# Kernel tuning notes

Measured on AMD Instinct MI355X. Metric: run time of the kernel, lower is better.

The kernel has to match this reference:

```python
import jax, jax.numpy as jnp
import numpy as np

N = 100000   # n_nodes
E = 1000000  # n_edges
B = 2000     # batch of interactions
K = 20       # n_neighbors
D = 172      # memory/node/edge/embedding dim
T = 172      # time encoding dim
MSG = 2 * D + D + T  # 688, identity message function
HEADS = 2


def setup_inputs() -> dict:
    key = jax.random.key(0)
    ks = jax.random.split(key, 32)
    g = lambda i, shape, fan: jax.random.normal(ks[i], shape, jnp.float32) / np.float32(np.sqrt(fan))
    inp = {}
    inp['memory'] = jax.random.normal(ks[0], (N, D), jnp.float32)
    inp['messages'] = jax.random.normal(ks[1], (N, MSG), jnp.float32)
    inp['edge_features'] = jax.random.normal(ks[2], (E, D), jnp.float32)
    inp['edge_times'] = jax.random.uniform(ks[3], (B,), jnp.float32) * 10000.0
    inp['neighbor_times'] = jax.random.uniform(ks[4], (3 * B, K), jnp.float32) * 10000.0
    # TimeEncode init: w = 1 / 10^linspace(0, 9, T)
    inp['time_w'] = jnp.asarray(1.0 / 10.0 ** np.linspace(0, 9, T), jnp.float32)
    inp['time_b'] = jnp.zeros((T,), jnp.float32)
    # GRUCell params
    inp['gru_w_ih'] = g(5, (3 * D, MSG), MSG)
    inp['gru_w_hh'] = g(6, (3 * D, D), D)
    inp['gru_b_ih'] = jnp.zeros((3 * D,), jnp.float32)
    inp['gru_b_hh'] = jnp.zeros((3 * D,), jnp.float32)
    # temporal attention params: query = [feat||time], key = [feat||edge||time]
    inp['w_q'] = g(7, (D, D + T), D + T)
    inp['w_k'] = g(8, (D, D + D + T), D + D + T)
    inp['w_v'] = g(9, (D, D + D + T), D + D + T)
    inp['w_o'] = g(10, (D, D), D)
    # MergeLayer(attn_out, src_feat)
    inp['merge_w1'] = g(11, (D, 2 * D), 2 * D)
    inp['merge_b1'] = jnp.zeros((D,), jnp.float32)
    inp['merge_w2'] = g(12, (D, D), D)
    inp['merge_b2'] = jnp.zeros((D,), jnp.float32)
    # affinity MergeLayer -> scalar score
    inp['aff_w1'] = g(13, (D, 2 * D), 2 * D)
    inp['aff_b1'] = jnp.zeros((D,), jnp.float32)
    inp['aff_w2'] = g(14, (1, D), D)
    inp['aff_b2'] = jnp.zeros((1,), jnp.float32)
    inp['source_nodes'] = jax.random.randint(ks[15], (B,), 0, N, jnp.int32)
    inp['destination_nodes'] = jax.random.randint(ks[16], (B,), 0, N, jnp.int32)
    inp['negative_nodes'] = jax.random.randint(ks[17], (B,), 0, N, jnp.int32)
    inp['neighbors'] = jax.random.randint(ks[18], (3 * B, K), 0, N, jnp.int32)
    inp['neighbor_edge_idxs'] = jax.random.randint(ks[19], (3 * B, K), 0, E, jnp.int32)
    return inp


def reference(memory, messages, edge_features, edge_times, neighbor_times,
              time_w, time_b, gru_w_ih, gru_w_hh, gru_b_ih, gru_b_hh,
              w_q, w_k, w_v, w_o, merge_w1, merge_b1, merge_w2, merge_b2,
              aff_w1, aff_b1, aff_w2, aff_b2,
              source_nodes, destination_nodes, negative_nodes,
              neighbors, neighbor_edge_idxs):
    d = memory.shape[1]
    dh = d // HEADS
    k_nbr = neighbors.shape[1]

    def time_enc(t):  # TimeEncode: cos(t * w + b)
        return jnp.cos(t[..., None] * time_w + time_b)

    # --- GRU memory update from aggregated ('last') messages ---
    gi = messages @ gru_w_ih.T + gru_b_ih          # [N, 3D]
    gh = memory @ gru_w_hh.T + gru_b_hh            # [N, 3D]
    i_r, i_z, i_n = jnp.split(gi, 3, axis=-1)
    h_r, h_z, h_n = jnp.split(gh, 3, axis=-1)
    r = jax.nn.sigmoid(i_r + h_r)
    z = jax.nn.sigmoid(i_z + h_z)
    n = jnp.tanh(i_n + r * h_n)
    mem_upd = (1.0 - z) * n + z * memory           # [N, D]

    # --- temporal graph attention embedding (1 layer) ---
    nodes = jnp.concatenate([source_nodes, destination_nodes, negative_nodes])  # [3B]
    ts = jnp.concatenate([edge_times, edge_times, edge_times])                  # [3B]
    m = nodes.shape[0]
    src_feat = mem_upd[nodes]                                                   # [3B, D]
    q_in = jnp.concatenate([src_feat, time_enc(jnp.zeros_like(ts))], axis=-1)   # [3B, D+T]
    nbr_feat = mem_upd[neighbors]                                               # [3B, K, D]
    e_feat = edge_features[neighbor_edge_idxs]                                  # [3B, K, D]
    dt = ts[:, None] - neighbor_times                                           # [3B, K]
    k_in = jnp.concatenate([nbr_feat, e_feat, time_enc(dt)], axis=-1)           # [3B, K, 2D+T]

    q = (q_in @ w_q.T).reshape(m, HEADS, dh)
    kk = (k_in @ w_k.T).reshape(m, k_nbr, HEADS, dh)
    vv = (k_in @ w_v.T).reshape(m, k_nbr, HEADS, dh)
    scores = jnp.einsum('nhd,nkhd->nhk', q, kk) / np.float32(np.sqrt(dh))
    valid = (neighbors > 0)[:, None, :]            # node 0 is the pad node
    scores = jnp.where(valid, scores, jnp.float32(-1e9))
    attn = jax.nn.softmax(scores, axis=-1)
    ctx = jnp.einsum('nhk,nkhd->nhd', attn, vv).reshape(m, d) @ w_o.T
    h1 = jax.nn.relu(jnp.concatenate([ctx, src_feat], axis=-1) @ merge_w1.T + merge_b1)
    emb = h1 @ merge_w2.T + merge_b2               # [3B, D]

    # --- affinity score on (src,dst) and (src,neg) pairs ---
    b = source_nodes.shape[0]
    s_emb, d_emb, n_emb = emb[:b], emb[b:2 * b], emb[2 * b:]
    s_cat = jnp.concatenate([s_emb, s_emb], axis=0)
    d_cat = jnp.concatenate([d_emb, n_emb], axis=0)
    ah = jax.nn.relu(jnp.concatenate([s_cat, d_cat], axis=-1) @ aff_w1.T + aff_b1)
    prob = jax.nn.sigmoid((ah @ aff_w2.T + aff_b2).squeeze(-1))  # [2B]
    return prob[:b], prob[b:]
```

## Files before the change

kernel.cpp:

```cpp
#include <hip/hip_runtime.h>
#include <math.h>

#define N_NODES 100000
#define BATCH   2000
#define KNBR    20
#define DF      172
#define MSGD    688
#define M3      6000
#define DH      86
#define KIN_D   516

#define KA      864
#define JP      768
#define KREAL   860
#define KSTEPS  (KA / 32)
#define NTILES_N ((N_NODES + 127) / 128)
#define NWG_GRU (NTILES_N * 6)

#define NKV     120000
#define KP_KV   544
#define JKV     384
#define KVS     352
#define NKV_TILES ((NKV + 127) / 128)

typedef __bf16 bf16x8 __attribute__((ext_vector_type(8)));
typedef __bf16 bf16x4 __attribute__((ext_vector_type(4)));
typedef float  f32x4  __attribute__((ext_vector_type(4)));

#define WPB_OFF   0
#define BP4_OFF   331776
#define WKV_OFF   332544
#define MU_OFF    436992
#define UNI_OFF   17636992
#define KV_OFF    UNI_OFF
#define QB_OFF    38756992
#define CAT_OFF   39286400
#define EMBB_OFF  40922752
#define MW1O_OFF  41812608
#define WQB_OFF   41842192
#define WM1B_OFF  41875984
#define WM2B_OFF  41909776
#define WAFFB_OFF 41928208
#define BM1P_OFF  41962000
#define BM2P_OFF  41962192
#define BAFFP_OFF 41962384
#define NODES_OFF 41962768

__device__ __forceinline__ float sigmoidf_(float x) { return 1.0f / (1.0f + expf(-x)); }

typedef __attribute__((address_space(1))) const void gvoid;
typedef __attribute__((address_space(3))) void svoid;
__device__ __forceinline__ void gl16(const void* g, void* l) {
    __builtin_amdgcn_global_load_lds((gvoid*)g, (svoid*)l, 16, 0, 0);
}

__global__ __launch_bounds__(256) void prep_kernel(
    const float* __restrict__ w_ih, const float* __restrict__ w_hh,
    const float* __restrict__ b_ih, const float* __restrict__ b_hh,
    __bf16* __restrict__ wpb, float* __restrict__ bp4)
{
    int idx = blockIdx.x * 256 + threadIdx.x;
    if (idx < JP * KA) {
        int j = idx / KA, k = idx - j * KA;
        int d = j >> 2, g = j & 3;
        float v = 0.f;
        if (d < DF) {
            if (g == 0) {
                if (k < MSGD) v = w_ih[d * MSGD + k];
                else if (k < KREAL) v = w_hh[d * DF + (k - MSGD)];
            } else if (g == 1) {
                if (k < MSGD) v = w_ih[(d + DF) * MSGD + k];
                else if (k < KREAL) v = w_hh[(d + DF) * DF + (k - MSGD)];
            } else if (g == 2) {
                if (k < MSGD) v = w_ih[(d + 2 * DF) * MSGD + k];
            } else {
                if (k >= MSGD && k < KREAL) v = w_hh[(d + 2 * DF) * DF + (k - MSGD)];
            }
        }
        wpb[idx] = (__bf16)v;
    }
    if (idx < JP) {
        int d = idx >> 2, g = idx & 3;
        float b = 0.f;
        if (d < DF) {
            if (g == 0) b = b_ih[d] + b_hh[d];
            else if (g == 1) b = b_ih[d + DF] + b_hh[d + DF];
            else if (g == 2) b = b_ih[d + 2 * DF];
            else            b = b_hh[d + 2 * DF];
        }
        bp4[idx] = b;
    }
}

__global__ __launch_bounds__(256) void prep_kv_kernel(
    const float* __restrict__ w_k, const float* __restrict__ w_v,
    __bf16* __restrict__ wkvb)
{
    int idx = blockIdx.x * 256 + threadIdx.x;
    if (idx < JKV * KP_KV) {
        int j = idx / KP_KV, k = idx - j * KP_KV;
        float v = 0.f;
        if (k < KIN_D) {
            if (j < DF) v = w_k[j * KIN_D + k];
            else if (j >= 192 && j < 192 + DF) v = w_v[(j - 192) * KIN_D + k];
        }
        wkvb[idx] = (__bf16)v;
    }
}

__global__ __launch_bounds__(256) void conv_kernel(
    const float* __restrict__ messages, const float* __restrict__ memory,
    __bf16* __restrict__ xb)
{
    const long total = (long)N_NODES * (KA / 8);
    for (long idx = (long)blockIdx.x * 256 + threadIdx.x; idx < total;
         idx += (long)gridDim.x * 256) {
        const int r  = (int)(idx / (KA / 8));
        const int k  = (int)(idx - (long)r * (KA / 8)) * 8;
        float f[8];
        if (k < MSGD) {
            const float4 a = *(const float4*)(messages + (size_t)r * MSGD + k);
            const float4 b = *(const float4*)(messages + (size_t)r * MSGD + k + 4);
            f[0]=a.x; f[1]=a.y; f[2]=a.z; f[3]=a.w;
            f[4]=b.x; f[5]=b.y; f[6]=b.z; f[7]=b.w;
        } else {
            const int o = k - MSGD;
            const float4 a = *(const float4*)(memory + (size_t)r * DF + o);
            float4 b = make_float4(0.f, 0.f, 0.f, 0.f);
            if (o <= 164) b = *(const float4*)(memory + (size_t)r * DF + o + 4);
            f[0]=a.x; f[1]=a.y; f[2]=a.z; f[3]=a.w;
            f[4]=b.x; f[5]=b.y; f[6]=b.z; f[7]=b.w;
        }
        bf16x8 v;
#pragma unroll
        for (int j = 0; j < 8; ++j) v[j] = (__bf16)f[j];
        *(bf16x8*)(xb + (size_t)r * KA + k) = v;
    }
}

__global__ __launch_bounds__(256) void mw1o_kernel(
    const float* __restrict__ merge_w1, const float* __restrict__ w_o,
    float* __restrict__ mw1o)
{
    int idx = blockIdx.x * 256 + threadIdx.x;
    if (idx >= DF * DF) return;
    int j = idx / DF, k = idx - j * DF;
    float s = 0.f;
    for (int c = 0; c < DF; ++c)
        s = fmaf(merge_w1[j * 344 + c], w_o[c * DF + k], s);
    mw1o[idx] = s;
}

__global__ __launch_bounds__(256) void prep_tail_kernel(
    const float* __restrict__ w_q, const float* __restrict__ mw1o,
    const float* __restrict__ merge_w1, const float* __restrict__ merge_w2,
    const float* __restrict__ aff_w1,
    const float* __restrict__ merge_b1, const float* __restrict__ merge_b2,
    const float* __restrict__ aff_b1,
    const int* __restrict__ src_nodes, const int* __restrict__ dst_nodes,
    const int* __restrict__ neg_nodes,
    __bf16* __restrict__ wqb, __bf16* __restrict__ wm1b,
    __bf16* __restrict__ wm2b, __bf16* __restrict__ waffb,
    float* __restrict__ bm1p, float* __restrict__ bm2p,
    float* __restrict__ baffp, int* __restrict__ nodes_cat)
{
    int idx = blockIdx.x * 256 + threadIdx.x;
    if (idx < 192 * 352) {
        int j = idx / 352, k = idx - j * 352;
        float vq = 0.f, vm = 0.f, va = 0.f;
        if (j < DF) {
            if (k < DF) {
                vq = w_q[j * 344 + k];
                vm = mw1o[j * DF + k];
                va = aff_w1[j * 344 + k];
            } else if (k >= 176 && k < 348) {
                vq = w_q[j * 344 + 172 + (k - 176)];
                vm = merge_w1[j * 344 + 172 + (k - 176)];
                va = aff_w1[j * 344 + 172 + (k - 176)];
            }
        }
        wqb[idx] = (__bf16)vq;
        wm1b[idx] = (__bf16)vm;
        waffb[idx] = (__bf16)va;
    }
    if (idx < 192 * 192) {
        int j = idx / 192, k = idx - j * 192;
        wm2b[idx] = (__bf16)((j < DF && k < DF) ? merge_w2[j * DF + k] : 0.f);
    }
    if (idx < 192) {
        bm1p[idx]  = (idx < DF) ? merge_b1[idx] : 0.f;
        bm2p[idx]  = (idx < DF) ? merge_b2[idx] : 0.f;
        baffp[idx] = (idx < DF) ? aff_b1[idx] : 0.f;
    }
    if (idx < 6016) {
        int i = min(idx, M3 - 1);
        int node;
        if (i < BATCH)          node = src_nodes[i];
        else if (i < 2 * BATCH) node = dst_nodes[i - BATCH];
        else                    node = neg_nodes[i - 2 * BATCH];
        nodes_cat[idx] = node;
    }
}

__global__ __launch_bounds__(256) void gru_mfma3_kernel(
    const __bf16* __restrict__ xb, const __bf16* __restrict__ wpb,
    const float* __restrict__ bp4, const float* __restrict__ memory,
    __bf16* __restrict__ mem_upd)
{
    __shared__ __align__(16) __bf16 Ws[3][128 * 32];
    __shared__ __align__(16) __bf16 Xs[3][128 * 32];

    const int t    = threadIdx.x;
    const int w    = t >> 6, lane = t & 63;
    const int lo   = lane & 15, hi = lane >> 4;
    const int wm   = w >> 1, wn = w & 1;

    const int orig = blockIdx.x;
    const int q = NWG_GRU >> 3, rr = NWG_GRU & 7;
    const int xcd = orig & 7, oidx = orig >> 3;
    const int wgid = (xcd < rr ? xcd * (q + 1) : rr * (q + 1) + (xcd - rr) * q) + oidx;
    const int m_tile = wgid % 6;
    const int n_tile = wgid / 6;
    const int n0 = n_tile * 128;
    const int j0 = m_tile * 128;

    const int srow  = lane >> 2;
    const int sslot = ((lane & 3) ^ ((lane >> 3) & 3)) * 8;

    f32x4 acc[4][4];
#pragma unroll
    for (int mi = 0; mi < 4; ++mi)
#pragma unroll
        for (int ni = 0; ni < 4; ++ni)
            acc[mi][ni] = (f32x4){0.f, 0.f, 0.f, 0.f};

    const __bf16* wbase = wpb + (size_t)j0 * KA;
    const __bf16* xbase = xb + (size_t)n0 * KA;

#define STAGE(buf, k0)                                                          \
    {                                                                           \
        _Pragma("unroll")                                                       \
        for (int qq = 0; qq < 2; ++qq) {                                        \
            const int lr = w * 32 + qq * 16 + srow;                             \
            gl16(wbase + (size_t)lr * KA + (k0) + sslot,                        \
                 &Ws[buf][(w * 32 + qq * 16) * 32]);                            \
            gl16(xbase + (size_t)lr * KA + (k0) + sslot,                        \
                 &Xs[buf][(w * 32 + qq * 16) * 32]);                            \
        }                                                                       \
    }

    STAGE(0, 0);
    STAGE(1, 32);

    const int fsa = (hi ^ ((lo >> 1) & 3)) * 8;
    for (int ks = 0; ks < KSTEPS; ++ks) {
        if (ks < KSTEPS - 1) {
            asm volatile("s_waitcnt vmcnt(4)" ::: "memory");
        } else {
            asm volatile("s_waitcnt vmcnt(0)" ::: "memory");
        }
        __builtin_amdgcn_s_barrier();
        if (ks + 2 < KSTEPS) STAGE((ks + 2) % 3, (ks + 2) * 32);

        const int bi = ks % 3;
        bf16x8 af[4], bx_[4];
#pragma unroll
        for (int i = 0; i < 4; ++i) {
            af[i]  = *(const bf16x8*)&Ws[bi][(wm * 64 + i * 16 + lo) * 32 + fsa];
            bx_[i] = *(const bf16x8*)&Xs[bi][(wn * 64 + i * 16 + lo) * 32 + fsa];
        }
#pragma unroll
        for (int mi = 0; mi < 4; ++mi)
#pragma unroll
            for (int ni = 0; ni < 4; ++ni)
                acc[mi][ni] = __builtin_amdgcn_mfma_f32_16x16x32_bf16(
                    af[mi], bx_[ni], acc[mi][ni], 0, 0, 0);
    }
#undef STAGE

    const int dbase = m_tile * 32 + wm * 16;
#pragma unroll
    for (int mi = 0; mi < 4; ++mi) {
        const int d = dbase + mi * 4 + hi;
        if (d >= DF) continue;
        const float4 b4 = *(const float4*)&bp4[4 * d];
#pragma unroll
        for (int ni = 0; ni < 4; ++ni) {
            const int n = n0 + wn * 64 + ni * 16 + lo;
            if (n >= N_NODES) continue;
            float sr  = acc[mi][ni][0] + b4.x;
            float sz  = acc[mi][ni][1] + b4.y;
            float gin = acc[mi][ni][2] + b4.z;
            float ghn = acc[mi][ni][3] + b4.w;
            float mem = memory[(size_t)n * DF + d];
            float rg  = sigmoidf_(sr);
            float zg  = sigmoidf_(sz);
            float nt  = tanhf(fmaf(rg, ghn, gin));
            mem_upd[(size_t)n * DF + d] = (__bf16)fmaf(zg, mem - nt, nt);
        }
    }
}

__global__ __launch_bounds__(256) void kv_gemm3_kernel(
    const __bf16* __restrict__ mem_upd, const float* __restrict__ edge_features,
    const float* __restrict__ edge_times, const float* __restrict__ neighbor_times,
    const float* __restrict__ time_w, const float* __restrict__ time_b,
    const int* __restrict__ neighbors, const int* __restrict__ nbr_eidx,
    const __bf16* __restrict__ wkvb, __bf16* __restrict__ kv)
{
    __shared__ __align__(16) __bf16 Ws[128][32];
    __shared__ __align__(16) __bf16 Xs[128][32];

    const int t    = threadIdx.x;
    const int w    = t >> 6, lane = t & 63;
    const int lo   = lane & 15, hi = lane >> 4;
    const int wm   = w >> 1, wn = w & 1;

    const int bx     = blockIdx.x;
    const int n_tile = bx / 3;
    const int m_tile = bx - n_tile * 3;
    const int n0     = n_tile * 128;
    const int j0     = m_tile * 128;

    const int xrow  = t >> 1, xhalf = t & 1;
    const int nr    = min(n0 + xrow, NKV - 1);
    const int nbr   = neighbors[nr];
    const int eidx  = nbr_eidx[nr];
    const float dt  = edge_times[(nr / KNBR) % BATCH] - neighbor_times[nr];
    const __bf16* mrow = mem_upd       + (size_t)nbr  * DF;
    const float*  erow = edge_features + (size_t)eidx * DF;
    const __bf16* wrow = wkvb + (size_t)(j0 + xrow) * KP_KV;

    f32x4 acc[4][4];
#pragma unroll
    for (int mi = 0; mi < 4; ++mi)
#pragma unroll
        for (int ni = 0; ni < 4; ++ni)
            acc[mi][ni] = (f32x4){0.f, 0.f, 0.f, 0.f};

#define LOADX(k0, xh, xf)                                                       \
    {                                                                           \
        _Pragma("unroll")                                                       \
        for (int c = 0; c < 4; ++c) {                                           \
            const int kb = (k0) + xhalf * 16 + c * 4;                           \
            if (kb < DF) {                                                      \
                xh[c] = *(const bf16x4*)(mrow + kb);                            \
            } else if (kb < 2 * DF) {                                           \
                xf[c] = *(const float4*)(erow + (kb - DF));                     \
            } else if (kb < KIN_D) {                                            \
                const float4 tw = *(const float4*)(time_w + (kb - 2 * DF));     \
                const float4 tb = *(const float4*)(time_b + (kb - 2 * DF));     \
                float4 v;                                                       \
                v.x = cosf(fmaf(dt, tw.x, tb.x));                               \
                v.y = cosf(fmaf(dt, tw.y, tb.y));                               \
                v.z = cosf(fmaf(dt, tw.z, tb.z));                               \
                v.w = cosf(fmaf(dt, tw.w, tb.w));                               \
                xf[c] = v;                                                      \
            } else {                                                            \
                xf[c] = make_float4(0.f, 0.f, 0.f, 0.f);                        \
            }                                                                   \
        }                                                                       \
    }

    bf16x4 xh[4];
    float4 xf[4];
    bf16x8 wp0, wp1;
    LOADX(0, xh, xf);
    wp0 = *(const bf16x8*)(wrow + xhalf * 16);
    wp1 = *(const bf16x8*)(wrow + xhalf * 16 + 8);

    for (int ks = 0; ks < KP_KV / 32; ++ks) {
        const int k0 = ks * 32;
        bf16x8 x0, x1;
#pragma unroll
        for (int c = 0; c < 4; ++c) {
            const int kb = k0 + xhalf * 16 + c * 4;
            __bf16 e0, e1, e2, e3;
            if (kb < DF) {
                e0 = xh[c][0]; e1 = xh[c][1]; e2 = xh[c][2]; e3 = xh[c][3];
            } else {
                e0 = (__bf16)xf[c].x; e1 = (__bf16)xf[c].y;
                e2 = (__bf16)xf[c].z; e3 = (__bf16)xf[c].w;
            }
            if (c < 2) { x0[c*4]=e0; x0[c*4+1]=e1; x0[c*4+2]=e2; x0[c*4+3]=e3; }
            else { x1[(c-2)*4]=e0; x1[(c-2)*4+1]=e1; x1[(c-2)*4+2]=e2; x1[(c-2)*4+3]=e3; }
        }
        *(bf16x8*)&Ws[xrow][xhalf * 16]     = wp0;
        *(bf16x8*)&Ws[xrow][xhalf * 16 + 8] = wp1;
        *(bf16x8*)&Xs[xrow][xhalf * 16]     = x0;
        *(bf16x8*)&Xs[xrow][xhalf * 16 + 8] = x1;

        if (ks + 1 < KP_KV / 32) {
            LOADX(k0 + 32, xh, xf);
            wp0 = *(const bf16x8*)(wrow + k0 + 32 + xhalf * 16);
            wp1 = *(const bf16x8*)(wrow + k0 + 32 + xhalf * 16 + 8);
        }

        asm volatile("s_waitcnt lgkmcnt(0)" ::: "memory");
        __builtin_amdgcn_s_barrier();

        bf16x8 af[4], bx_[4];
#pragma unroll
        for (int i = 0; i < 4; ++i) {
            af[i]  = *(const bf16x8*)&Ws[wm * 64 + i * 16 + lo][hi * 8];
            bx_[i] = *(const bf16x8*)&Xs[wn * 64 + i * 16 + lo][hi * 8];
        }
#pragma unroll
        for (int mi = 0; mi < 4; ++mi)
#pragma unroll
            for (int ni = 0; ni < 4; ++ni)
                acc[mi][ni] = __builtin_amdgcn_mfma_f32_16x16x32_bf16(
                    af[mi], bx_[ni], acc[mi][ni], 0, 0, 0);

        __builtin_amdgcn_s_barrier();
    }
#undef LOADX

#pragma unroll
    for (int mi = 0; mi < 4; ++mi) {
        const int jb = j0 + wm * 64 + mi * 16 + hi * 4;
        int off;
        if (jb + 3 < DF)                 off = jb;
        else if (jb >= 192 && jb < 361)  off = jb - 16;
        else continue;
#pragma unroll
        for (int ni = 0; ni < 4; ++ni) {
            const int n = n0 + wn * 64 + ni * 16 + lo;
            if (n >= NKV) continue;
            bf16x4 o;
            o[0] = (__bf16)acc[mi][ni][0];
            o[1] = (__bf16)acc[mi][ni][1];
            o[2] = (__bf16)acc[mi][ni][2];
            o[3] = (__bf16)acc[mi][ni][3];
            *(bf16x4*)(kv + (size_t)n * KVS + off) = o;
        }
    }
}

__global__ __launch_bounds__(256) void q_gemm_kernel(
    const __bf16* __restrict__ wqb, const __bf16* __restrict__ mem_upd,
    const float* __restrict__ time_b, const int* __restrict__ nodes_cat,
    __bf16* __restrict__ qbuf)
{
    __shared__ __align__(16) __bf16 Ws[128][32];
    __shared__ __align__(16) __bf16 Xs[128][32];

    const int t    = threadIdx.x;
    const int w    = t >> 6, lane = t & 63;
    const int lo   = lane & 15, hi = lane >> 4;
    const int wm   = w >> 1, wn = w & 1;

    const int n_tile = blockIdx.x >> 1;
    const int j0     = (blockIdx.x & 1) * 64;
    const int n0     = n_tile * 128;

    const int xrow  = t >> 1, xhalf = t & 1;
    const int nr    = min(n0 + xrow, M3 - 1);
    const __bf16* mrow = mem_upd + (size_t)nodes_cat[nr] * DF;
    const __bf16* wrow = wqb + (size_t)(j0 + xrow) * 352;

    f32x4 acc[4][4];
#pragma unroll
    for (int mi = 0; mi < 4; ++mi)
#pragma unroll
        for (int ni = 0; ni < 4; ++ni)
            acc[mi][ni] = (f32x4){0.f, 0.f, 0.f, 0.f};

    for (int k0 = 0; k0 < 352; k0 += 32) {
        bf16x8 w0 = *(const bf16x8*)(wrow + k0 + xhalf * 16);
        bf16x8 w1 = *(const bf16x8*)(wrow + k0 + xhalf * 16 + 8);
        bf16x8 x0, x1;
#pragma unroll
        for (int c = 0; c < 4; ++c) {
            const int b = k0 + xhalf * 16 + c * 4;
            __bf16 e0, e1, e2, e3;
            if (b + 3 < DF) {
                bf16x4 h = *(const bf16x4*)(mrow + b);
                e0 = h[0]; e1 = h[1]; e2 = h[2]; e3 = h[3];
            } else if (b >= 176 && b < 348) {
                const float4 tb = *(const float4*)(time_b + (b - 176));
                e0 = (__bf16)cosf(tb.x); e1 = (__bf16)cosf(tb.y);
                e2 = (__bf16)cosf(tb.z); e3 = (__bf16)cosf(tb.w);
            } else {
                e0 = e1 = e2 = e3 = (__bf16)0.f;
            }
            if (c < 2) { x0[c*4]=e0; x0[c*4+1]=e1; x0[c*4+2]=e2; x0[c*4+3]=e3; }
            else { x1[(c-2)*4]=e0; x1[(c-2)*4+1]=e1; x1[(c-2)*4+2]=e2; x1[(c-2)*4+3]=e3; }
        }
        *(bf16x8*)&Ws[xrow][xhalf * 16]     = w0;
        *(bf16x8*)&Ws[xrow][xhalf * 16 + 8] = w1;
        *(bf16x8*)&Xs[xrow][xhalf * 16]     = x0;
        *(bf16x8*)&Xs[xrow][xhalf * 16 + 8] = x1;
        __syncthreads();

        bf16x8 af[4], bx_[4];
#pragma unroll
        for (int i = 0; i < 4; ++i) {
            af[i]  = *(const bf16x8*)&Ws[wm * 64 + i * 16 + lo][hi * 8];
            bx_[i] = *(const bf16x8*)&Xs[wn * 64 + i * 16 + lo][hi * 8];
        }
#pragma unroll
        for (int mi = 0; mi < 4; ++mi)
#pragma unroll
            for (int ni = 0; ni < 4; ++ni)
                acc[mi][ni] = __builtin_amdgcn_mfma_f32_16x16x32_bf16(
                    af[mi], bx_[ni], acc[mi][ni], 0, 0, 0);
        __syncthreads();
    }

#pragma unroll
    for (int mi = 0; mi < 4; ++mi) {
        const int jb = j0 + wm * 64 + mi * 16 + hi * 4;
        if (jb + 3 >= 176) continue;
#pragma unroll
        for (int ni = 0; ni < 4; ++ni) {
            const int n = n0 + wn * 64 + ni * 16 + lo;
            if (n >= M3) continue;
            bf16x4 o;
            o[0]=(__bf16)acc[mi][ni][0]; o[1]=(__bf16)acc[mi][ni][1];
            o[2]=(__bf16)acc[mi][ni][2]; o[3]=(__bf16)acc[mi][ni][3];
            *(bf16x4*)(qbuf + (size_t)n * 176 + jb) = o;
        }
    }
}

__global__ __launch_bounds__(256) void attn_mid_kernel(
    const __bf16* __restrict__ mem_upd, const __bf16* __restrict__ kv,
    const __bf16* __restrict__ qb, const int* __restrict__ neighbors,
    const int* __restrict__ nodes_cat, __bf16* __restrict__ cat)
{
    __shared__ __align__(16) __bf16 kvs[KNBR][KVS];
    __shared__ float qs[176];
    __shared__ float scl[2][KNBR];
    __shared__ float attnl[2][KNBR];
    __shared__ int   nbrs[KNBR];

    const int i = blockIdx.x;
    const int t = threadIdx.x;

    if (t < KNBR) nbrs[t] = neighbors[i * KNBR + t];
    if (t < 176) qs[t] = (float)qb[(size_t)i * 176 + t];
    {
        const uint4* src = (const uint4*)(kv + (size_t)i * KNBR * KVS);
        uint4* dst = (uint4*)&kvs[0][0];
        for (int idx = t; idx < KNBR * KVS / 8; idx += 256) dst[idx] = src[idx];
    }
    __syncthreads();

    if (t < 2 * KNBR) {
        int h = t / KNBR, kn = t - h * KNBR;
        float s = 0.f;
#pragma unroll 2
        for (int j = 0; j < DH; ++j)
            s = fmaf(qs[h * DH + j], (float)kvs[kn][h * DH + j], s);
        s /= sqrtf((float)DH);
        scl[h][kn] = (nbrs[kn] > 0) ? s : -1e9f;
    }
    __syncthreads();
    if (t < 2) {
        float m = -INFINITY;
        for (int kn = 0; kn < KNBR; ++kn) m = fmaxf(m, scl[t][kn]);
        float se = 0.f;
        for (int kn = 0; kn < KNBR; ++kn) se += expf(scl[t][kn] - m);
        float inv = 1.f / se;
        for (int kn = 0; kn < KNBR; ++kn) attnl[t][kn] = expf(scl[t][kn] - m) * inv;
    }
    __syncthreads();
    if (t < DF) {
        int h = t / DH;
        float cx = 0.f;
#pragma unroll
        for (int kn = 0; kn < KNBR; ++kn)
            cx = fmaf(attnl[h][kn], (float)kvs[kn][176 + t], cx);
        cat[(size_t)i * 352 + t] = (__bf16)cx;
        cat[(size_t)i * 352 + 176 + t] = mem_upd[(size_t)nodes_cat[i] * DF + t];
    }
    if (t < 4) {
        cat[(size_t)i * 352 + 172 + t] = (__bf16)0.f;
        cat[(size_t)i * 352 + 348 + t] = (__bf16)0.f;
    }
}

__global__ __launch_bounds__(256) void merge_emb_kernel(
    const __bf16* __restrict__ cat, const __bf16* __restrict__ wm1b,
    const __bf16* __restrict__ wm2b, const float* __restrict__ bm1p,
    const float* __restrict__ bm2p, __bf16* __restrict__ embb)
{
    __shared__ __align__(16) __bf16 Ws[192 * 32];
    __shared__ __align__(16) __bf16 Xs[128 * 32];
    __shared__ __align__(16) __bf16 h1[128 * 200];

    const int t    = threadIdx.x;
    const int w    = t >> 6, lane = t & 63;
    const int lo   = lane & 15, hi = lane >> 4;
    const int wm   = w >> 1, wn = w & 1;
    const int n0   = blockIdx.x * 128;

    const int srow  = lane >> 2;
    const int sslot = ((lane & 3) ^ ((lane >> 3) & 3)) * 8;
    const int fsa   = (hi ^ ((lo >> 1) & 3)) * 8;

    f32x4 acc[6][4];
#pragma unroll
    for (int mi = 0; mi < 6; ++mi)
#pragma unroll
        for (int ni = 0; ni < 4; ++ni)
            acc[mi][ni] = (f32x4){0.f, 0.f, 0.f, 0.f};

    for (int k0 = 0; k0 < 352; k0 += 32) {
#pragma unroll
        for (int qq = 0; qq < 3; ++qq) {
            const int jr = w * 48 + qq * 16 + srow;
            gl16(wm1b + (size_t)jr * 352 + k0 + sslot, &Ws[(w * 48 + qq * 16) * 32]);
        }
#pragma unroll
        for (int qq = 0; qq < 2; ++qq) {
            const int r = w * 32 + qq * 16 + srow;
            const int nr = min(n0 + r, M3 - 1);
            gl16(cat + (size_t)nr * 352 + k0 + sslot, &Xs[(w * 32 + qq * 16) * 32]);
        }
        asm volatile("s_waitcnt vmcnt(0)" ::: "memory");
        __syncthreads();

        bf16x8 af[6], bx_[4];
#pragma unroll
        for (int i = 0; i < 6; ++i)
            af[i] = *(const bf16x8*)&Ws[(wm * 96 + i * 16 + lo) * 32 + fsa];
#pragma unroll
        for (int i = 0; i < 4; ++i)
            bx_[i] = *(const bf16x8*)&Xs[(wn * 64 + i * 16 + lo) * 32 + fsa];
#pragma unroll
        for (int mi = 0; mi < 6; ++mi)
#pragma unroll
            for (int ni = 0; ni < 4; ++ni)
                acc[mi][ni] = __builtin_amdgcn_mfma_f32_16x16x32_bf16(
                    af[mi], bx_[ni], acc[mi][ni], 0, 0, 0);
        __syncthreads();
    }

#pragma unroll
    for (int mi = 0; mi < 6; ++mi) {
        const int jb = wm * 96 + mi * 16 + hi * 4;
        const float4 b4 = *(const float4*)(bm1p + jb);
#pragma unroll
        for (int ni = 0; ni < 4; ++ni) {
            const int nl = wn * 64 + ni * 16 + lo;
            bf16x4 o;
            o[0] = (__bf16)fmaxf(acc[mi][ni][0] + b4.x, 0.f);
            o[1] = (__bf16)fmaxf(acc[mi][ni][1] + b4.y, 0.f);
            o[2] = (__bf16)fmaxf(acc[mi][ni][2] + b4.z, 0.f);
            o[3] = (__bf16)fmaxf(acc[mi][ni][3] + b4.w, 0.f);
            *(bf16x4*)&h1[nl * 200 + jb] = o;
        }
    }
    __syncthreads();

    f32x4 acc2[6][4];
#pragma unroll
    for (int mi = 0; mi < 6; ++mi)
#pragma unroll
        for (int ni = 0; ni < 4; ++ni)
            acc2[mi][ni] = (f32x4){0.f, 0.f, 0.f, 0.f};

    for (int k0 = 0; k0 < 192; k0 += 32) {
#pragma unroll
        for (int qq = 0; qq < 3; ++qq) {
            const int jr = w * 48 + qq * 16 + srow;
            gl16(wm2b + (size_t)jr * 192 + k0 + sslot, &Ws[(w * 48 + qq * 16) * 32]);
        }
        asm volatile("s_waitcnt vmcnt(0)" ::: "memory");
        __syncthreads();

        bf16x8 af[6], bx_[4];
#pragma unroll
        for (int i = 0; i < 6; ++i)
            af[i] = *(const bf16x8*)&Ws[(wm * 96 + i * 16 + lo) * 32 + fsa];
#pragma unroll
        for (int i = 0; i < 4; ++i)
            bx_[i] = *(const bf16x8*)&h1[(wn * 64 + i * 16 + lo) * 200 + k0 + hi * 8];
#pragma unroll
        for (int mi = 0; mi < 6; ++mi)
#pragma unroll
            for (int ni = 0; ni < 4; ++ni)
                acc2[mi][ni] = __builtin_amdgcn_mfma_f32_16x16x32_bf16(
                    af[mi], bx_[ni], acc2[mi][ni], 0, 0, 0);
        __syncthreads();
    }

#pragma unroll
    for (int mi = 0; mi < 6; ++mi) {
        const int jb = wm * 96 + mi * 16 + hi * 4;
        if (jb + 3 >= 176) continue;
        const float4 b4 = *(const float4*)(bm2p + jb);
#pragma unroll
        for (int ni = 0; ni < 4; ++ni) {
            const int n = n0 + wn * 64 + ni * 16 + lo;
            if (n >= M3) continue;
            bf16x4 o;
            o[0] = (__bf16)(acc2[mi][ni][0] + b4.x);
            o[1] = (__bf16)(acc2[mi][ni][1] + b4.y);
            o[2] = (__bf16)(acc2[mi][ni][2] + b4.z);
            o[3] = (__bf16)(acc2[mi][ni][3] + b4.w);
            *(bf16x4*)(embb + (size_t)n * 176 + jb) = o;
        }
    }
}

__global__ __launch_bounds__(256) void aff_fused_kernel(
    const __bf16* __restrict__ embb, const __bf16* __restrict__ waffb,
    const float* __restrict__ baffp, const float* __restrict__ aff_w2,
    const float* __restrict__ aff_b2, float* __restrict__ out)
{
    __shared__ __align__(16) __bf16 Ws[192 * 32];
    __shared__ __align__(16) __bf16 Xs[128 * 32];
    __shared__ float sred[2][2][4][16];

    const int t    = threadIdx.x;
    const int w    = t >> 6, lane = t & 63;
    const int lo   = lane & 15, hi = lane >> 4;
    const int wm   = w >> 1, wn = w & 1;
    const int n0   = blockIdx.x * 128;

    const int srow  = lane >> 2;
    const int sslot = ((lane & 3) ^ ((lane >> 3) & 3)) * 8;
    const int fsa   = (hi ^ ((lo >> 1) & 3)) * 8;

    f32x4 acc[6][4];
#pragma unroll
    for (int mi = 0; mi < 6; ++mi)
#pragma unroll
        for (int ni = 0; ni < 4; ++ni)
            acc[mi][ni] = (f32x4){0.f, 0.f, 0.f, 0.f};

    for (int k0 = 0; k0 < 352; k0 += 32) {
#pragma unroll
        for (int qq = 0; qq < 3; ++qq) {
            const int jr = w * 48 + qq * 16 + srow;
            gl16(waffb + (size_t)jr * 352 + k0 + sslot, &Ws[(w * 48 + qq * 16) * 32]);
        }
#pragma unroll
        for (int qq = 0; qq < 2; ++qq) {
            const int r = w * 32 + qq * 16 + srow;
            const int nr = min(n0 + r, 2 * BATCH - 1);
            const int s  = (nr < BATCH) ? nr : nr - BATCH;
            const int col = k0 + sslot;
            const __bf16* src = (col < 176)
                ? embb + (size_t)s * 176 + col
                : embb + (size_t)(nr + BATCH) * 176 + (col - 176);
            gl16(src, &Xs[(w * 32 + qq * 16) * 32]);
        }
        asm volatile("s_waitcnt vmcnt(0)" ::: "memory");
        __syncthreads();

        bf16x8 af[6], bx_[4];
#pragma unroll
        for (int i = 0; i < 6; ++i)
            af[i] = *(const bf16x8*)&Ws[(wm * 96 + i * 16 + lo) * 32 + fsa];
#pragma unroll
        for (int i = 0; i < 4; ++i)
            bx_[i] = *(const bf16x8*)&Xs[(wn * 64 + i * 16 + lo) * 32 + fsa];
#pragma unroll
        for (int mi = 0; mi < 6; ++mi)
#pragma unroll
            for (int ni = 0; ni < 4; ++ni)
                acc[mi][ni] = __builtin_amdgcn_mfma_f32_16x16x32_bf16(
                    af[mi], bx_[ni], acc[mi][ni], 0, 0, 0);
        __syncthreads();
    }

    float ps[4] = {0.f, 0.f, 0.f, 0.f};
#pragma unroll
    for (int mi = 0; mi < 6; ++mi) {
        const int jb = wm * 96 + mi * 16 + hi * 4;
#pragma unroll
        for (int r = 0; r < 4; ++r) {
            const int j = jb + r;
            const float w2v = (j < DF) ? aff_w2[j] : 0.f;
            const float bb  = baffp[j];
#pragma unroll
            for (int ni = 0; ni < 4; ++ni)
                ps[ni] += fmaxf(acc[mi][ni][r] + bb, 0.f) * w2v;
        }
    }
#pragma unroll
    for (int ni = 0; ni < 4; ++ni) {
        ps[ni] += __shfl_xor(ps[ni], 16, 64);
        ps[ni] += __shfl_xor(ps[ni], 32, 64);
    }
    if (hi == 0) {
#pragma unroll
        for (int ni = 0; ni < 4; ++ni) sred[wm][wn][ni][lo] = ps[ni];
    }
    __syncthreads();
    if (t < 128) {
        const int n = n0 + t;
        if (n < 2 * BATCH) {
            const int wn2 = t >> 6, ni = (t >> 4) & 3, lo2 = t & 15;
            float s = sred[0][wn2][ni][lo2] + sred[1][wn2][ni][lo2] + aff_b2[0];
            out[n] = 1.f / (1.f + expf(-s));
        }
    }
}

extern "C" void kernel_launch(void* const* d_in, const int* in_sizes, int n_in,
                              void* d_out, int out_size, void* d_ws, size_t ws_size,
                              hipStream_t stream)
{
    (void)in_sizes; (void)n_in; (void)out_size; (void)ws_size;
    const float* memory         = (const float*)d_in[0];
    const float* messages       = (const float*)d_in[1];
    const float* edge_features  = (const float*)d_in[2];
    const float* edge_times     = (const float*)d_in[3];
    const float* neighbor_times = (const float*)d_in[4];
    const float* time_w         = (const float*)d_in[5];
    const float* time_b         = (const float*)d_in[6];
    const float* gru_w_ih       = (const float*)d_in[7];
    const float* gru_w_hh       = (const float*)d_in[8];
    const float* gru_b_ih       = (const float*)d_in[9];
    const float* gru_b_hh       = (const float*)d_in[10];
    const float* w_q            = (const float*)d_in[11];
    const float* w_k            = (const float*)d_in[12];
    const float* w_v            = (const float*)d_in[13];
    const float* w_o            = (const float*)d_in[14];
    const float* merge_w1       = (const float*)d_in[15];
    const float* merge_b1       = (const float*)d_in[16];
    const float* merge_w2       = (const float*)d_in[17];
    const float* merge_b2       = (const float*)d_in[18];
    const float* aff_w1         = (const float*)d_in[19];
    const float* aff_b1         = (const float*)d_in[20];
    const float* aff_w2         = (const float*)d_in[21];
    const float* aff_b2         = (const float*)d_in[22];
    const int* src_nodes        = (const int*)d_in[23];
    const int* dst_nodes        = (const int*)d_in[24];
    const int* neg_nodes        = (const int*)d_in[25];
    const int* neighbors        = (const int*)d_in[26];
    const int* nbr_eidx         = (const int*)d_in[27];

    float* ws       = (float*)d_ws;
    __bf16* wpb     = (__bf16*)(ws + WPB_OFF);
    float* bp4      = ws + BP4_OFF;
    __bf16* wkvb    = (__bf16*)(ws + WKV_OFF);
    __bf16* mem_upd = (__bf16*)(ws + MU_OFF);
    __bf16* xbuf    = (__bf16*)(ws + UNI_OFF);
    __bf16* kv      = (__bf16*)(ws + KV_OFF);
    __bf16* qbuf    = (__bf16*)(ws + QB_OFF);
    __bf16* cat     = (__bf16*)(ws + CAT_OFF);
    __bf16* embb    = (__bf16*)(ws + EMBB_OFF);
    float* mw1o     = ws + MW1O_OFF;
    __bf16* wqb     = (__bf16*)(ws + WQB_OFF);
    __bf16* wm1b    = (__bf16*)(ws + WM1B_OFF);
    __bf16* wm2b    = (__bf16*)(ws + WM2B_OFF);
    __bf16* waffb   = (__bf16*)(ws + WAFFB_OFF);
    float* bm1p     = ws + BM1P_OFF;
    float* bm2p     = ws + BM2P_OFF;
    float* baffp    = ws + BAFFP_OFF;
    int*   nodes_cat= (int*)(ws + NODES_OFF);
    float* out      = (float*)d_out;

    prep_kernel<<<(JP * KA + 255) / 256, 256, 0, stream>>>(
        gru_w_ih, gru_w_hh, gru_b_ih, gru_b_hh, wpb, bp4);
    prep_kv_kernel<<<(JKV * KP_KV + 255) / 256, 256, 0, stream>>>(w_k, w_v, wkvb);
    conv_kernel<<<2048, 256, 0, stream>>>(messages, memory, xbuf);
    gru_mfma3_kernel<<<NWG_GRU, 256, 0, stream>>>(xbuf, wpb, bp4, memory, mem_upd);
    mw1o_kernel<<<(DF * DF + 255) / 256, 256, 0, stream>>>(merge_w1, w_o, mw1o);
    prep_tail_kernel<<<(192 * 352 + 255) / 256, 256, 0, stream>>>(
        w_q, mw1o, merge_w1, merge_w2, aff_w1, merge_b1, merge_b2, aff_b1,
        src_nodes, dst_nodes, neg_nodes,
        wqb, wm1b, wm2b, waffb, bm1p, bm2p, baffp, nodes_cat);
    kv_gemm3_kernel<<<NKV_TILES * 3, 256, 0, stream>>>(
        mem_upd, edge_features, edge_times, neighbor_times, time_w, time_b,
        neighbors, nbr_eidx, wkvb, kv);
    q_gemm_kernel<<<47 * 2, 256, 0, stream>>>(wqb, mem_upd, time_b, nodes_cat, qbuf);
    attn_mid_kernel<<<M3, 256, 0, stream>>>(
        mem_upd, kv, qbuf, neighbors, nodes_cat, cat);
    merge_emb_kernel<<<47, 256, 0, stream>>>(cat, wm1b, wm2b, bm1p, bm2p, embb);
    aff_fused_kernel<<<32, 256, 0, stream>>>(embb, waffb, baffp, aff_w2, aff_b2, out);
}
```

Baseline: 722.6 us.

## Split KV gather into a separate kernel and use 8-wave async-LDS GEMMs

The GRU GEMM goes from 4 to 8 waves per 128x128 tile, so each wave holds a 64x32 slice, and the LDS swizzle is adjusted to match. The fused gather+KV GEMM is split in two. A new kernel materialises the bf16 K-input rows (neighbor memory, edge features, cosine time encoding) into a workspace buffer. A KV GEMM then streams that buffer with global_load_lds triple buffering and an XCD-aware block remap, instead of register staging with two barriers per step. This aims to raise occupancy and overlap memory loads with MFMA work. The cost is an extra write and read of a ~130 MB intermediate and one more kernel launch.

```diff
diff --git a/kernel.cpp b/kernel.cpp
--- a/kernel.cpp
+++ b/kernel.cpp
@@ -22,6 +22,9 @@
 #define JKV     384
 #define KVS     352
 #define NKV_TILES ((NKV + 127) / 128)
+#define NKV_ROWS (NKV_TILES * 128)
+#define NWG_KV  (NKV_TILES * 3)
+#define KSTEPS_KV (KP_KV / 32)
 
 typedef __bf16 bf16x8 __attribute__((ext_vector_type(8)));
 typedef __bf16 bf16x4 __attribute__((ext_vector_type(4)));
@@ -45,6 +48,7 @@
 #define BM2P_OFF  41962192
 #define BAFFP_OFF 41962384
 #define NODES_OFF 41962768
+#define KIN_OFF   42000000
 
 __device__ __forceinline__ float sigmoidf_(float x) { return 1.0f / (1.0f + expf(-x)); }
 
@@ -202,7 +206,7 @@
     }
 }
 
-__global__ __launch_bounds__(256) void gru_mfma3_kernel(
+__global__ __launch_bounds__(512) void gru_mfma5_kernel(
     const __bf16* __restrict__ xb, const __bf16* __restrict__ wpb,
     const float* __restrict__ bp4, const float* __restrict__ memory,
     __bf16* __restrict__ mem_upd)
@@ -213,7 +217,8 @@
     const int t    = threadIdx.x;
     const int w    = t >> 6, lane = t & 63;
     const int lo   = lane & 15, hi = lane >> 4;
-    const int wm   = w >> 1, wn = w & 1;
+    const int wm   = w & 1;
+    const int wn   = w >> 1;
 
     const int orig = blockIdx.x;
     const int q = NWG_GRU >> 3, rr = NWG_GRU & 7;
@@ -225,13 +230,13 @@
     const int j0 = m_tile * 128;
 
     const int srow  = lane >> 2;
-    const int sslot = ((lane & 3) ^ ((lane >> 3) & 3)) * 8;
-
-    f32x4 acc[4][4];
+    const int sslot = ((lane & 3) ^ ((srow >> 1) & 3)) * 8;
+
+    f32x4 acc[4][2];
 #pragma unroll
     for (int mi = 0; mi < 4; ++mi)
 #pragma unroll
-        for (int ni = 0; ni < 4; ++ni)
+        for (int ni = 0; ni < 2; ++ni)
             acc[mi][ni] = (f32x4){0.f, 0.f, 0.f, 0.f};
 
     const __bf16* wbase = wpb + (size_t)j0 * KA;
@@ -239,14 +244,9 @@
 
 #define STAGE(buf, k0)                                                          \
     {                                                                           \
-        _Pragma("unroll")                                                       \
-        for (int qq = 0; qq < 2; ++qq) {                                        \
-            const int lr = w * 32 + qq * 16 + srow;                             \
-            gl16(wbase + (size_t)lr * KA + (k0) + sslot,                        \
-                 &Ws[buf][(w * 32 + qq * 16) * 32]);                            \
-            gl16(xbase + (size_t)lr * KA + (k0) + sslot,                        \
-                 &Xs[buf][(w * 32 + qq * 16) * 32]);                            \
-        }                                                                       \
+        const int lr = w * 16 + srow;                                           \
+        gl16(wbase + (size_t)lr * KA + (k0) + sslot, &Ws[buf][(w * 16) * 32]);  \
+        gl16(xbase + (size_t)lr * KA + (k0) + sslot, &Xs[buf][(w * 16) * 32]);  \
     }
 
     STAGE(0, 0);
@@ -255,7 +255,7 @@
     const int fsa = (hi ^ ((lo >> 1) & 3)) * 8;
     for (int ks = 0; ks < KSTEPS; ++ks) {
         if (ks < KSTEPS - 1) {
-            asm volatile("s_waitcnt vmcnt(4)" ::: "memory");
+            asm volatile("s_waitcnt vmcnt(2)" ::: "memory");
         } else {
             asm volatile("s_waitcnt vmcnt(0)" ::: "memory");
         }
@@ -263,16 +263,17 @@
         if (ks + 2 < KSTEPS) STAGE((ks + 2) % 3, (ks + 2) * 32);
 
         const int bi = ks % 3;
-        bf16x8 af[4], bx_[4];
-#pragma unroll
-        for (int i = 0; i < 4; ++i) {
+        bf16x8 af[4], bx_[2];
+#pragma unroll
+        for (int i = 0; i < 4; ++i)
             af[i]  = *(const bf16x8*)&Ws[bi][(wm * 64 + i * 16 + lo) * 32 + fsa];
-            bx_[i] = *(const bf16x8*)&Xs[bi][(wn * 64 + i * 16 + lo) * 32 + fsa];
-        }
+#pragma unroll
+        for (int i = 0; i < 2; ++i)
+            bx_[i] = *(const bf16x8*)&Xs[bi][(wn * 32 + i * 16 + lo) * 32 + fsa];
 #pragma unroll
         for (int mi = 0; mi < 4; ++mi)
 #pragma unroll
-            for (int ni = 0; ni < 4; ++ni)
+            for (int ni = 0; ni < 2; ++ni)
                 acc[mi][ni] = __builtin_amdgcn_mfma_f32_16x16x32_bf16(
                     af[mi], bx_[ni], acc[mi][ni], 0, 0, 0);
     }
@@ -285,8 +286,8 @@
         if (d >= DF) continue;
         const float4 b4 = *(const float4*)&bp4[4 * d];
 #pragma unroll
-        for (int ni = 0; ni < 4; ++ni) {
-            const int n = n0 + wn * 64 + ni * 16 + lo;
+        for (int ni = 0; ni < 2; ++ni) {
+            const int n = n0 + wn * 32 + ni * 16 + lo;
             if (n >= N_NODES) continue;
             float sr  = acc[mi][ni][0] + b4.x;
             float sz  = acc[mi][ni][1] + b4.y;
@@ -301,120 +302,114 @@
     }
 }
 
-__global__ __launch_bounds__(256) void kv_gemm3_kernel(
+__global__ __launch_bounds__(256) void kin_build_kernel(
     const __bf16* __restrict__ mem_upd, const float* __restrict__ edge_features,
     const float* __restrict__ edge_times, const float* __restrict__ neighbor_times,
     const float* __restrict__ time_w, const float* __restrict__ time_b,
     const int* __restrict__ neighbors, const int* __restrict__ nbr_eidx,
-    const __bf16* __restrict__ wkvb, __bf16* __restrict__ kv)
-{
-    __shared__ __align__(16) __bf16 Ws[128][32];
-    __shared__ __align__(16) __bf16 Xs[128][32];
+    __bf16* __restrict__ kin)
+{
+    const long total = (long)NKV_ROWS * 136;
+    for (long idx = (long)blockIdx.x * 256 + threadIdx.x; idx < total;
+         idx += (long)gridDim.x * 256) {
+        const int r  = (int)(idx / 136);
+        const int c  = (int)(idx - (long)r * 136) * 4;
+        const int rc = min(r, NKV - 1);
+        bf16x4 o;
+        if (c < DF) {
+            const int nbr = neighbors[rc];
+            o = *(const bf16x4*)(mem_upd + (size_t)nbr * DF + c);
+        } else if (c < 2 * DF) {
+            const int eidx = nbr_eidx[rc];
+            const float4 v = *(const float4*)(edge_features + (size_t)eidx * DF + (c - DF));
+            o[0] = (__bf16)v.x; o[1] = (__bf16)v.y;
+            o[2] = (__bf16)v.z; o[3] = (__bf16)v.w;
+        } else if (c < KIN_D) {
+            const float dt = edge_times[(rc / KNBR) % BATCH] - neighbor_times[rc];
+            const float4 tw = *(const float4*)(time_w + (c - 2 * DF));
+            const float4 tb = *(const float4*)(time_b + (c - 2 * DF));
+            o[0] = (__bf16)cosf(fmaf(dt, tw.x, tb.x));
+            o[1] = (__bf16)cosf(fmaf(dt, tw.y, tb.y));
+            o[2] = (__bf16)cosf(fmaf(dt, tw.z, tb.z));
+            o[3] = (__bf16)cosf(fmaf(dt, tw.w, tb.w));
+        } else {
+            o[0] = o[1] = o[2] = o[3] = (__bf16)0.f;
+        }
+        *(bf16x4*)(kin + (size_t)r * KP_KV + c) = o;
+    }
+}
+
+__global__ __launch_bounds__(512) void kv_gemm4_kernel(
+    const __bf16* __restrict__ kin, const __bf16* __restrict__ wkvb,
+    __bf16* __restrict__ kv)
+{
+    __shared__ __align__(16) __bf16 Ws[3][128 * 32];
+    __shared__ __align__(16) __bf16 Xs[3][128 * 32];
 
     const int t    = threadIdx.x;
     const int w    = t >> 6, lane = t & 63;
     const int lo   = lane & 15, hi = lane >> 4;
-    const int wm   = w >> 1, wn = w & 1;
-
-    const int bx     = blockIdx.x;
-    const int n_tile = bx / 3;
-    const int m_tile = bx - n_tile * 3;
-    const int n0     = n_tile * 128;
-    const int j0     = m_tile * 128;
-
-    const int xrow  = t >> 1, xhalf = t & 1;
-    const int nr    = min(n0 + xrow, NKV - 1);
-    const int nbr   = neighbors[nr];
-    const int eidx  = nbr_eidx[nr];
-    const float dt  = edge_times[(nr / KNBR) % BATCH] - neighbor_times[nr];
-    const __bf16* mrow = mem_upd       + (size_t)nbr  * DF;
-    const float*  erow = edge_features + (size_t)eidx * DF;
-    const __bf16* wrow = wkvb + (size_t)(j0 + xrow) * KP_KV;
-
-    f32x4 acc[4][4];
+    const int wm   = w & 1;
+    const int wn   = w >> 1;
+
+    const int orig = blockIdx.x;
+    const int q = NWG_KV >> 3, rr = NWG_KV & 7;
+    const int xcd = orig & 7, oidx = orig >> 3;
+    const int wgid = (xcd < rr ? xcd * (q + 1) : rr * (q + 1) + (xcd - rr) * q) + oidx;
+    const int m_tile = wgid % 3;
+    const int n_tile = wgid / 3;
+    const int n0 = n_tile * 128;
+    const int j0 = m_tile * 128;
+
+    const int srow  = lane >> 2;
+    const int sslot = ((lane & 3) ^ ((srow >> 1) & 3)) * 8;
+
+    f32x4 acc[4][2];
 #pragma unroll
     for (int mi = 0; mi < 4; ++mi)
 #pragma unroll
-        for (int ni = 0; ni < 4; ++ni)
+        for (int ni = 0; ni < 2; ++ni)
             acc[mi][ni] = (f32x4){0.f, 0.f, 0.f, 0.f};
 
-#define LOADX(k0, xh, xf)                                                       \
-    {                                                                           \
-        _Pragma("unroll")                                                       \
-        for (int c = 0; c < 4; ++c) {                                           \
-            const int kb = (k0) + xhalf * 16 + c * 4;                           \
-            if (kb < DF) {                                                      \
-                xh[c] = *(const bf16x4*)(mrow + kb);                            \
-            } else if (kb < 2 * DF) {                                           \
-                xf[c] = *(const float4*)(erow + (kb - DF));                     \
-            } else if (kb < KIN_D) {                                            \
-                const float4 tw = *(const float4*)(time_w + (kb - 2 * DF));     \
-                const float4 tb = *(const float4*)(time_b + (kb - 2 * DF));     \
-                float4 v;                                                       \
-                v.x = cosf(fmaf(dt, tw.x, tb.x));                               \
-                v.y = cosf(fmaf(dt, tw.y, tb.y));                               \
-                v.z = cosf(fmaf(dt, tw.z, tb.z));                               \
-                v.w = cosf(fmaf(dt, tw.w, tb.w));                               \
-                xf[c] = v;                                                      \
-            } else {                                                            \
-                xf[c] = make_float4(0.f, 0.f, 0.f, 0.f);                        \
-            }                                                                   \
-        }                                                                       \
-    }
-
-    bf16x4 xh[4];
-    float4 xf[4];
-    bf16x8 wp0, wp1;
-    LOADX(0, xh, xf);
-    wp0 = *(const bf16x8*)(wrow + xhalf * 16);
-    wp1 = *(const bf16x8*)(wrow + xhalf * 16 + 8);
-
-    for (int ks = 0; ks < KP_KV / 32; ++ks) {
-        const int k0 = ks * 32;
-        bf16x8 x0, x1;
-#pragma unroll
-        for (int c = 0; c < 4; ++c) {
-            const int kb = k0 + xhalf * 16 + c * 4;
-            __bf16 e0, e1, e2, e3;
-            if (kb < DF) {
-                e0 = xh[c][0]; e1 = xh[c][1]; e2 = xh[c][2]; e3 = xh[c][3];
-            } else {
-                e0 = (__bf16)xf[c].x; e1 = (__bf16)xf[c].y;
-                e2 = (__bf16)xf[c].z; e3 = (__bf16)xf[c].w;
-            }
-            if (c < 2) { x0[c*4]=e0; x0[c*4+1]=e1; x0[c*4+2]=e2; x0[c*4+3]=e3; }
-            else { x1[(c-2)*4]=e0; x1[(c-2)*4+1]=e1; x1[(c-2)*4+2]=e2; x1[(c-2)*4+3]=e3; }
-        }
-        *(bf16x8*)&Ws[xrow][xhalf * 16]     = wp0;
-        *(bf16x8*)&Ws[xrow][xhalf * 16 + 8] = wp1;
-        *(bf16x8*)&Xs[xrow][xhalf * 16]     = x0;
-        *(bf16x8*)&Xs[xrow][xhalf * 16 + 8] = x1;
-
-        if (ks + 1 < KP_KV / 32) {
-            LOADX(k0 + 32, xh, xf);
-            wp0 = *(const bf16x8*)(wrow + k0 + 32 + xhalf * 16);
-            wp1 = *(const bf16x8*)(wrow + k0 + 32 + xhalf * 16 + 8);
-        }
-
-        asm volatile("s_waitcnt lgkmcnt(0)" ::: "memory");
+    const __bf16* wbase = wkvb + (size_t)j0 * KP_KV;
+    const __bf16* xbase = kin + (size_t)n0 * KP_KV;
+
+#define STAGE(buf, k0)                                                           \
+    {                                                                            \
+        const int lr = w * 16 + srow;                                            \
+        gl16(wbase + (size_t)lr * KP_KV + (k0) + sslot, &Ws[buf][(w * 16) * 32]);\
+        gl16(xbase + (size_t)lr * KP_KV + (k0) + sslot, &Xs[buf][(w * 16) * 32]);\
+    }
+
+    STAGE(0, 0);
+    STAGE(1, 32);
+
+    const int fsa = (hi ^ ((lo >> 1) & 3)) * 8;
+    for (int ks = 0; ks < KSTEPS_KV; ++ks) {
+        if (ks < KSTEPS_KV - 1) {
+            asm volatile("s_waitcnt vmcnt(2)" ::: "memory");
+        } else {
+            asm volatile("s_waitcnt vmcnt(0)" ::: "memory");
+        }
         __builtin_amdgcn_s_barrier();
-
-        bf16x8 af[4], bx_[4];
-#pragma unroll
-        for (int i = 0; i < 4; ++i) {
-            af[i]  = *(const bf16x8*)&Ws[wm * 64 + i * 16 + lo][hi * 8];
-            bx_[i] = *(const bf16x8*)&Xs[wn * 64 + i * 16 + lo][hi * 8];
-        }
+        if (ks + 2 < KSTEPS_KV) STAGE((ks + 2) % 3, (ks + 2) * 32);
+
+        const int bi = ks % 3;
+        bf16x8 af[4], bx_[2];
+#pragma unroll
+        for (int i = 0; i < 4; ++i)
+            af[i]  = *(const bf16x8*)&Ws[bi][(wm * 64 + i * 16 + lo) * 32 + fsa];
+#pragma unroll
+        for (int i = 0; i < 2; ++i)
+            bx_[i] = *(const bf16x8*)&Xs[bi][(wn * 32 + i * 16 + lo) * 32 + fsa];
 #pragma unroll
         for (int mi = 0; mi < 4; ++mi)
 #pragma unroll
-            for (int ni = 0; ni < 4; ++ni)
+            for (int ni = 0; ni < 2; ++ni)
                 acc[mi][ni] = __builtin_amdgcn_mfma_f32_16x16x32_bf16(
                     af[mi], bx_[ni], acc[mi][ni], 0, 0, 0);
-
-        __builtin_amdgcn_s_barrier();
-    }
-#undef LOADX
+    }
+#undef STAGE
 
 #pragma unroll
     for (int mi = 0; mi < 4; ++mi) {
@@ -424,8 +419,8 @@
         else if (jb >= 192 && jb < 361)  off = jb - 16;
         else continue;
 #pragma unroll
-        for (int ni = 0; ni < 4; ++ni) {
-            const int n = n0 + wn * 64 + ni * 16 + lo;
+        for (int ni = 0; ni < 2; ++ni) {
+            const int n = n0 + wn * 32 + ni * 16 + lo;
             if (n >= NKV) continue;
             bf16x4 o;
             o[0] = (__bf16)acc[mi][ni][0];
@@ -855,21 +850,23 @@
     float* bm2p     = ws + BM2P_OFF;
     float* baffp    = ws + BAFFP_OFF;
     int*   nodes_cat= (int*)(ws + NODES_OFF);
+    __bf16* kin     = (__bf16*)(ws + KIN_OFF);
     float* out      = (float*)d_out;
 
     prep_kernel<<<(JP * KA + 255) / 256, 256, 0, stream>>>(
         gru_w_ih, gru_w_hh, gru_b_ih, gru_b_hh, wpb, bp4);
     prep_kv_kernel<<<(JKV * KP_KV + 255) / 256, 256, 0, stream>>>(w_k, w_v, wkvb);
     conv_kernel<<<2048, 256, 0, stream>>>(messages, memory, xbuf);
-    gru_mfma3_kernel<<<NWG_GRU, 256, 0, stream>>>(xbuf, wpb, bp4, memory, mem_upd);
+    gru_mfma5_kernel<<<NWG_GRU, 512, 0, stream>>>(xbuf, wpb, bp4, memory, mem_upd);
     mw1o_kernel<<<(DF * DF + 255) / 256, 256, 0, stream>>>(merge_w1, w_o, mw1o);
     prep_tail_kernel<<<(192 * 352 + 255) / 256, 256, 0, stream>>>(
         w_q, mw1o, merge_w1, merge_w2, aff_w1, merge_b1, merge_b2, aff_b1,
         src_nodes, dst_nodes, neg_nodes,
         wqb, wm1b, wm2b, waffb, bm1p, bm2p, baffp, nodes_cat);
-    kv_gemm3_kernel<<<NKV_TILES * 3, 256, 0, stream>>>(
+    kin_build_kernel<<<2048, 256, 0, stream>>>(
         mem_upd, edge_features, edge_times, neighbor_times, time_w, time_b,
-        neighbors, nbr_eidx, wkvb, kv);
+        neighbors, nbr_eidx, kin);
+    kv_gemm4_kernel<<<NWG_KV, 512, 0, stream>>>(kin, wkvb, kv);
     q_gemm_kernel<<<47 * 2, 256, 0, stream>>>(wqb, mem_upd, time_b, nodes_cat, qbuf);
     attn_mid_kernel<<<M3, 256, 0, stream>>>(
         mem_upd, kv, qbuf, neighbors, nodes_cat, cat);
```

Measured after the change: 644.6 us. 10.8% less time.
